# Performance work log

Measured on AMD Instinct MI355X. Metric: run time of the kernel, lower is better.

## Reference

```python
import jax, jax.numpy as jnp
import numpy as np


def setup_inputs() -> dict:
    key = jax.random.key(0)
    k1, k2, k3, k4 = jax.random.split(key, 4)
    B, T, C, H = 8, 2048, 1024, 64
    x = jax.random.normal(k1, (B, T, C), dtype=jnp.float32)
    Wq = jax.random.normal(k2, (C, H), dtype=jnp.float32) * (C ** -0.5)
    Wk = jax.random.normal(k3, (C, H), dtype=jnp.float32) * (C ** -0.5)
    Wv = jax.random.normal(k4, (C, H), dtype=jnp.float32) * (C ** -0.5)
    return {"x": x, "Wq": Wq, "Wk": Wk, "Wv": Wv}


def reference(x, Wq, Wk, Wv):
    # x: [B,T,C]; Wq/Wk/Wv: [C,H] (nn.Linear bias=False => x @ W)
    B, T, C = x.shape
    H = Wq.shape[-1]
    q = jnp.einsum('btc,ch->bth', x, Wq)
    k = jnp.einsum('btc,ch->bth', x, Wk)
    v = jnp.einsum('btc,ch->bth', x, Wv)
    scale = H ** -0.5
    att = jnp.einsum('bqh,bkh->bqk', q, k) * scale  # [B,T,T]
    causal = jnp.tril(jnp.ones((T, T), dtype=bool))
    att = jnp.where(causal, att, -jnp.inf)
    att = jax.nn.softmax(att, axis=-1)
    out = jnp.einsum('bqk,bkh->bqh', att, v)  # [B,T,H]
    return out
```

## Files before the change

kernel.cpp:

```cpp
#include <hip/hip_runtime.h>
#include <hip/hip_bf16.h>
#include <math.h>

#define BB 8
#define TT 2048
#define CC 1024
#define HH 64
#define BT (BB * TT)

typedef __attribute__((ext_vector_type(8))) short short8;
typedef __attribute__((ext_vector_type(4))) float floatx4;

static __device__ inline ushort f2bf(float f) {
    __hip_bfloat16 h = __float2bfloat16(f);
    return *reinterpret_cast<ushort*>(&h);
}
static __device__ inline unsigned int f2bf2(float lo, float hi) {
    __hip_bfloat162 h = __float22bfloat162_rn(make_float2(lo, hi));
    return *reinterpret_cast<unsigned int*>(&h);
}
static __device__ inline float bf2f(ushort u) {
    union { unsigned int i; float f; } c;
    c.i = ((unsigned int)u) << 16;
    return c.f;
}

__global__ __launch_bounds__(256) void wprep_kernel(
    const float* __restrict__ Wq, const float* __restrict__ Wk,
    const float* __restrict__ Wv, ushort* __restrict__ WbT)
{
    __shared__ float ws_[64 * 65];
    const int m  = blockIdx.x >> 4;
    const int kb = (blockIdx.x & 15) * 64;
    const float* W = (m == 0) ? Wq : (m == 1) ? Wk : Wv;
    const int t  = threadIdx.x;
    const int lr = t >> 4, lc = (t & 15) * 4;
    #pragma unroll
    for (int i = 0; i < 4; ++i) {
        const int row = lr + i * 16;
        float4 v = *(const float4*)&W[(size_t)(kb + row) * HH + lc];
        ws_[row * 65 + lc + 0] = v.x; ws_[row * 65 + lc + 1] = v.y;
        ws_[row * 65 + lc + 2] = v.z; ws_[row * 65 + lc + 3] = v.w;
    }
    __syncthreads();
    const int n = t & 63, kseg = t >> 6;
    union { ushort s[16]; uint4 q[2]; } u;
    #pragma unroll
    for (int j = 0; j < 16; ++j)
        u.s[j] = f2bf(ws_[(kseg * 16 + j) * 65 + n]);
    ushort* dst = &WbT[(size_t)(m * 64 + n) * 1024 + kb + kseg * 16];
    *(uint4*)&dst[0] = u.q[0];
    *(uint4*)&dst[8] = u.q[1];
}

__global__ __launch_bounds__(256, 2) void qkv_kernel(
    const float* __restrict__ x, const ushort* __restrict__ WbT,
    ushort* __restrict__ qb, ushort* __restrict__ kbS, ushort* __restrict__ vS)
{
    const int t    = threadIdx.x;
    const int w    = t >> 6;
    const int lane = t & 63;
    const int l16  = lane & 15;
    const int quad = lane >> 4;

    const int rows0 = blockIdx.x * 32 + (w >> 1) * 16;
    const int ct0   = (w & 1) * 6;

    const float* xr = &x[(size_t)(rows0 + l16) * CC + quad * 8];
    const ushort* wb = &WbT[(size_t)l16 * 1024 + quad * 8];

    floatx4 acc[6];
    #pragma unroll
    for (int c = 0; c < 6; ++c) acc[c] = (floatx4){0.f, 0.f, 0.f, 0.f};

    float4 xcA[2][2], xcB[2][2];
    #pragma unroll
    for (int p = 0; p < 2; ++p) {
        xcA[p][0] = *(const float4*)&xr[p * 32 + 0];
        xcA[p][1] = *(const float4*)&xr[p * 32 + 4];
        xcB[p][0] = *(const float4*)&xr[64 + p * 32 + 0];
        xcB[p][1] = *(const float4*)&xr[64 + p * 32 + 4];
    }

    short8 afA[2][6], afB[2][6];
    #pragma unroll
    for (int p = 0; p < 2; ++p)
        #pragma unroll
        for (int c = 0; c < 6; ++c)
            afA[p][c] = *(const short8*)&wb[(size_t)(ct0 + c) * 16384 + p * 32];

    auto body = [&](int it, float4 (&xc)[2][2], short8 (&aCur)[2][6], short8 (&aNxt)[2][6]) {
        short8 bx[2];
        #pragma unroll
        for (int p = 0; p < 2; ++p) {
            union { unsigned int u[4]; short8 s; } cv;
            cv.u[0] = f2bf2(xc[p][0].x, xc[p][0].y);
            cv.u[1] = f2bf2(xc[p][0].z, xc[p][0].w);
            cv.u[2] = f2bf2(xc[p][1].x, xc[p][1].y);
            cv.u[3] = f2bf2(xc[p][1].z, xc[p][1].w);
            bx[p] = cv.s;
        }
        if (it + 2 < 16) {
            #pragma unroll
            for (int p = 0; p < 2; ++p) {
                xc[p][0] = *(const float4*)&xr[(it + 2) * 64 + p * 32 + 0];
                xc[p][1] = *(const float4*)&xr[(it + 2) * 64 + p * 32 + 4];
            }
        }
        if (it + 1 < 16) {
            #pragma unroll
            for (int p = 0; p < 2; ++p)
                #pragma unroll
                for (int c = 0; c < 6; ++c)
                    aNxt[p][c] = *(const short8*)&wb[(size_t)(ct0 + c) * 16384
                                                     + (it + 1) * 64 + p * 32];
        }
        __builtin_amdgcn_s_setprio(1);
        #pragma unroll
        for (int p = 0; p < 2; ++p)
            #pragma unroll
            for (int c = 0; c < 6; ++c)
                acc[c] = __builtin_amdgcn_mfma_f32_16x16x32_bf16(aCur[p][c], bx[p], acc[c], 0, 0, 0);
        __builtin_amdgcn_s_setprio(0);
    };

    #pragma unroll 1
    for (int it2 = 0; it2 < 16; it2 += 4) {
        body(it2 + 0, xcA, afA, afB);
        body(it2 + 1, xcB, afB, afA);
        body(it2 + 2, xcA, afA, afB);
        body(it2 + 3, xcB, afB, afA);
    }

    const size_t tile = (size_t)(rows0 >> 6) * 4096;
    #pragma unroll
    for (int c = 0; c < 6; ++c) {
        const int ct    = ct0 + c;
        const int mtype = ct >> 2;
        const int nn    = ct & 3;
        if (mtype == 0) {
            uint2 u;
            u.x = f2bf2(acc[c][0] * 0.125f, acc[c][1] * 0.125f);
            u.y = f2bf2(acc[c][2] * 0.125f, acc[c][3] * 0.125f);
            *(uint2*)&qb[(size_t)(rows0 + l16) * HH + nn * 16 + quad * 4] = u;
        } else if (mtype == 1) {
            const int ckey  = (rows0 >> 4) & 3;
            const int p     = nn >> 1;
            const int quadP = (nn * 2 + (quad >> 1)) & 3;
            const int j0    = (quad & 1) * 4;
            uint2 u;
            u.x = f2bf2(acc[c][0], acc[c][1]);
            u.y = f2bf2(acc[c][2], acc[c][3]);
            *(uint2*)&kbS[tile + (size_t)((ckey * 2 + p) * 64 + quadP * 16 + l16) * 8 + j0] = u;
        } else {
            const int pv = (rows0 >> 5) & 1;
            const int qv = ((rows0 >> 4) & 1) * 2 + (l16 >> 3);
            const int jv = l16 & 7;
            #pragma unroll
            for (int reg = 0; reg < 4; ++reg)
                vS[tile + (size_t)((nn * 2 + pv) * 64 + qv * 16 + quad * 4 + reg) * 8 + jv]
                    = f2bf(acc[c][reg]);
        }
    }
}

__global__ __launch_bounds__(256) void attn_kernel(
    const ushort* __restrict__ qb, const ushort* __restrict__ kbS,
    const ushort* __restrict__ vS, ushort* __restrict__ Opart,
    float* __restrict__ ml)
{
    __shared__ __align__(16) ushort P[4][16 * 72];

    const int t    = threadIdx.x;
    const int w    = t >> 6;
    const int lane = t & 63;
    const int l16  = lane & 15;
    const int quad = lane >> 4;

    const int b   = blockIdx.x & 7;
    const int idx = blockIdx.x >> 3;
    int qt, part, np;
    if (idx < 32)      { qt = 31 - (idx >> 2); part = idx & 3; np = 4; }
    else if (idx < 56) { const int u = idx - 32; const int g = u / 3;
                         qt = 23 - g; part = u - g * 3; np = 3; }
    else if (idx < 72) { const int u = idx - 56; qt = 15 - (u >> 1); part = u & 1; np = 2; }
    else               { qt = 7 - (idx - 72); part = 0; np = 1; }
    const int ntiles = qt + 1;
    const int ktb = (part * ntiles) / np;
    const int kte = ((part + 1) * ntiles) / np;

    const ushort* ktile0 = kbS + (size_t)(b * 32) * 4096;
    const ushort* vtile0 = vS  + (size_t)(b * 32) * 4096;

    short8 qf[2];
    {
        const ushort* qrow = qb + ((size_t)b * TT + qt * 64 + w * 16) * HH;
        qf[0] = *(const short8*)&qrow[l16 * HH + quad * 8];
        qf[1] = *(const short8*)&qrow[l16 * HH + 32 + quad * 8];
    }
    short8 ones;
    #pragma unroll
    for (int i = 0; i < 8; ++i) ones[i] = (short)0x3F80;

    floatx4 o[4], osum;
    #pragma unroll
    for (int c = 0; c < 4; ++c) o[c] = (floatx4){0.f, 0.f, 0.f, 0.f};
    osum = (floatx4){0.f, 0.f, 0.f, 0.f};

    ushort* Pw = &P[w][0];

    for (int kt = ktb; kt < kte; ++kt) {
        const ushort* kg = ktile0 + (size_t)kt * 4096;
        const ushort* vg = vtile0 + (size_t)kt * 4096;

        short8 kf[4][2];
        #pragma unroll
        for (int c = 0; c < 4; ++c)
            #pragma unroll
            for (int p = 0; p < 2; ++p)
                kf[c][p] = *(const short8*)&kg[(size_t)(((c * 2 + p) * 64) + lane) * 8];

        floatx4 s[4];
        #pragma unroll
        for (int c = 0; c < 4; ++c) s[c] = (floatx4){0.f, 0.f, 0.f, 0.f};
        __builtin_amdgcn_s_setprio(1);
        #pragma unroll
        for (int c = 0; c < 4; ++c)
            #pragma unroll
            for (int p = 0; p < 2; ++p)
                s[c] = __builtin_amdgcn_mfma_f32_16x16x32_bf16(kf[c][p], qf[p], s[c], 0, 0, 0);
        __builtin_amdgcn_s_setprio(0);

        short8 vf[4][2];
        #pragma unroll
        for (int c = 0; c < 4; ++c)
            #pragma unroll
            for (int p = 0; p < 2; ++p)
                vf[c][p] = *(const short8*)&vg[(size_t)(((c * 2 + p) * 64) + lane) * 8];

        if (kt == ntiles - 1) {
            const int key0 = kt * 64 + quad * 4;
            const int qrow = qt * 64 + w * 16 + l16;
            #pragma unroll
            for (int c = 0; c < 4; ++c)
                #pragma unroll
                for (int reg = 0; reg < 4; ++reg)
                    if (key0 + c * 16 + reg > qrow) s[c][reg] = -1e30f;
        }

        #pragma unroll
        for (int c = 0; c < 4; ++c) {
            uint2 u;
            u.x = f2bf2(__expf(s[c][0]), __expf(s[c][1]));
            u.y = f2bf2(__expf(s[c][2]), __expf(s[c][3]));
            *(uint2*)&Pw[l16 * 72 + c * 16 + quad * 4] = u;
        }

        short8 pf[2];
        pf[0] = *(const short8*)&Pw[l16 * 72 + quad * 8];
        pf[1] = *(const short8*)&Pw[l16 * 72 + 32 + quad * 8];

        __builtin_amdgcn_s_setprio(1);
        #pragma unroll
        for (int p = 0; p < 2; ++p) {
            #pragma unroll
            for (int c = 0; c < 4; ++c)
                o[c] = __builtin_amdgcn_mfma_f32_16x16x32_bf16(pf[p], vf[c][p], o[c], 0, 0, 0);
            osum = __builtin_amdgcn_mfma_f32_16x16x32_bf16(pf[p], ones, osum, 0, 0, 0);
        }
        __builtin_amdgcn_s_setprio(0);
    }

    const size_t ub = (size_t)blockIdx.x * 4096;
    const int rbase = w * 16 + quad * 4;
    #pragma unroll
    for (int c = 0; c < 4; ++c) {
        uint2 u;
        u.x = f2bf2(o[c][0], o[c][1]);
        u.y = f2bf2(o[c][2], o[c][3]);
        *(uint2*)&Opart[ub + (size_t)(c * 16 + l16) * 64 + rbase] = u;
    }
    if (l16 == 0) {
        #pragma unroll
        for (int reg = 0; reg < 4; ++reg)
            ml[(size_t)blockIdx.x * 64 + rbase + reg] = osum[reg];
    }
}

__global__ __launch_bounds__(256) void merge_kernel(
    const ushort* __restrict__ Opart, const float* __restrict__ ml,
    float* __restrict__ out)
{
    const int t    = threadIdx.x;
    const int gw   = blockIdx.x * 4 + (t >> 6);
    const int lane = t & 63;
    const int b    = gw >> 8;
    const int v    = gw & 255;
    const int qt   = v >> 3;
    const int oct  = v & 7;

    int base, np;
    if (qt >= 24)      { base = (31 - qt) * 4;      np = 4; }
    else if (qt >= 16) { base = 32 + (23 - qt) * 3; np = 3; }
    else if (qt >= 8)  { base = 56 + (15 - qt) * 2; np = 2; }
    else               { base = 72 + (7 - qt);      np = 1; }

    float* obase = out + ((size_t)b * TT + qt * 64) * HH;

    #pragma unroll
    for (int rg = 0; rg < 2; ++rg) {
        const int row0 = oct * 8 + rg * 4;
        float dx = 0.f, dy = 0.f, dz = 0.f, dw = 0.f;
        float ax = 0.f, ay = 0.f, az = 0.f, aw = 0.f;
        for (int p = 0; p < np; ++p) {
            const int unit = (base + p) * 8 + b;
            float4 d = *(const float4*)&ml[(size_t)unit * 64 + row0];
            dx += d.x; dy += d.y; dz += d.z; dw += d.w;
            ushort4 ov = *(const ushort4*)&Opart[(size_t)unit * 4096 + lane * 64 + row0];
            ax += bf2f(ov.x); ay += bf2f(ov.y); az += bf2f(ov.z); aw += bf2f(ov.w);
        }
        obase[(size_t)(row0 + 0) * HH + lane] = ax / dx;
        obase[(size_t)(row0 + 1) * HH + lane] = ay / dy;
        obase[(size_t)(row0 + 2) * HH + lane] = az / dz;
        obase[(size_t)(row0 + 3) * HH + lane] = aw / dw;
    }
}

extern "C" void kernel_launch(void* const* d_in, const int* in_sizes, int n_in,
                              void* d_out, int out_size, void* d_ws, size_t ws_size,
                              hipStream_t stream)
{
    (void)in_sizes; (void)n_in; (void)out_size; (void)ws_size;
    const float* x  = (const float*)d_in[0];
    const float* Wq = (const float*)d_in[1];
    const float* Wk = (const float*)d_in[2];
    const float* Wv = (const float*)d_in[3];
    float* outp = (float*)d_out;

    char* base = (char*)d_ws;
    ushort* WbT   = (ushort*)(base);
    ushort* qbuf  = (ushort*)(base + 393216);
    ushort* kbS   = qbuf + (size_t)BT * HH;
    ushort* vSb   = kbS + (size_t)BT * HH;
    ushort* Opart = vSb + (size_t)BT * HH;
    float*  ml    = (float*)((char*)Opart + (size_t)640 * 4096 * 2);

    wprep_kernel<<<dim3(48),  256, 0, stream>>>(Wq, Wk, Wv, WbT);
    qkv_kernel  <<<dim3(512), 256, 0, stream>>>(x, WbT, qbuf, kbS, vSb);
    attn_kernel <<<dim3(640), 256, 0, stream>>>(qbuf, kbS, vSb, Opart, ml);
    merge_kernel<<<dim3(512), 256, 0, stream>>>(Opart, ml, outp);
}
```

Before: 165.2 us.

## Split QKV projection work across more blocks with fewer accumulators per wave

Each block of the QKV projection now covers 16 rows instead of 32, and each wave computes 3 column tiles instead of 6, so the grid doubles to 1024 blocks. The launch bound asks for 4 blocks per SM instead of 2. The explicit double-buffered register prefetch of weight fragments and the two-stage x prefetch are replaced by a simple loop that loads weights each iteration and prefetches x one step ahead. The aim is to hide memory latency through higher occupancy rather than software pipelining. The cost is that each x row is now read by four waves in one block instead of two, and the weights are read by twice as many blocks.

```diff
diff --git a/kernel.cpp b/kernel.cpp
--- a/kernel.cpp
+++ b/kernel.cpp
@@ -53,7 +53,7 @@
     *(uint4*)&dst[8] = u.q[1];
 }
 
-__global__ __launch_bounds__(256, 2) void qkv_kernel(
+__global__ __launch_bounds__(256, 4) void qkv_kernel(
     const float* __restrict__ x, const ushort* __restrict__ WbT,
     ushort* __restrict__ qb, ushort* __restrict__ kbS, ushort* __restrict__ vS)
 {
@@ -63,33 +63,33 @@
     const int l16  = lane & 15;
     const int quad = lane >> 4;
 
-    const int rows0 = blockIdx.x * 32 + (w >> 1) * 16;
-    const int ct0   = (w & 1) * 6;
+    const int rows0 = blockIdx.x * 16;
+    const int ct0   = w * 3;
 
     const float* xr = &x[(size_t)(rows0 + l16) * CC + quad * 8];
     const ushort* wb = &WbT[(size_t)l16 * 1024 + quad * 8];
 
-    floatx4 acc[6];
-    #pragma unroll
-    for (int c = 0; c < 6; ++c) acc[c] = (floatx4){0.f, 0.f, 0.f, 0.f};
-
-    float4 xcA[2][2], xcB[2][2];
+    floatx4 acc[3];
+    #pragma unroll
+    for (int c = 0; c < 3; ++c) acc[c] = (floatx4){0.f, 0.f, 0.f, 0.f};
+
+    float4 xc[2][2];
     #pragma unroll
     for (int p = 0; p < 2; ++p) {
-        xcA[p][0] = *(const float4*)&xr[p * 32 + 0];
-        xcA[p][1] = *(const float4*)&xr[p * 32 + 4];
-        xcB[p][0] = *(const float4*)&xr[64 + p * 32 + 0];
-        xcB[p][1] = *(const float4*)&xr[64 + p * 32 + 4];
-    }
-
-    short8 afA[2][6], afB[2][6];
-    #pragma unroll
-    for (int p = 0; p < 2; ++p)
-        #pragma unroll
-        for (int c = 0; c < 6; ++c)
-            afA[p][c] = *(const short8*)&wb[(size_t)(ct0 + c) * 16384 + p * 32];
-
-    auto body = [&](int it, float4 (&xc)[2][2], short8 (&aCur)[2][6], short8 (&aNxt)[2][6]) {
+        xc[p][0] = *(const float4*)&xr[p * 32 + 0];
+        xc[p][1] = *(const float4*)&xr[p * 32 + 4];
+    }
+
+    #pragma unroll 4
+    for (int it = 0; it < 16; ++it) {
+        short8 af[2][3];
+        #pragma unroll
+        for (int p = 0; p < 2; ++p)
+            #pragma unroll
+            for (int c = 0; c < 3; ++c)
+                af[p][c] = *(const short8*)&wb[(size_t)(ct0 + c) * 16384
+                                               + it * 64 + p * 32];
+
         short8 bx[2];
         #pragma unroll
         for (int p = 0; p < 2; ++p) {
@@ -100,41 +100,27 @@
             cv.u[3] = f2bf2(xc[p][1].z, xc[p][1].w);
             bx[p] = cv.s;
         }
-        if (it + 2 < 16) {
+
+        if (it + 1 < 16) {
             #pragma unroll
             for (int p = 0; p < 2; ++p) {
-                xc[p][0] = *(const float4*)&xr[(it + 2) * 64 + p * 32 + 0];
-                xc[p][1] = *(const float4*)&xr[(it + 2) * 64 + p * 32 + 4];
+                xc[p][0] = *(const float4*)&xr[(it + 1) * 64 + p * 32 + 0];
+                xc[p][1] = *(const float4*)&xr[(it + 1) * 64 + p * 32 + 4];
             }
         }
-        if (it + 1 < 16) {
-            #pragma unroll
-            for (int p = 0; p < 2; ++p)
-                #pragma unroll
-                for (int c = 0; c < 6; ++c)
-                    aNxt[p][c] = *(const short8*)&wb[(size_t)(ct0 + c) * 16384
-                                                     + (it + 1) * 64 + p * 32];
-        }
+
         __builtin_amdgcn_s_setprio(1);
         #pragma unroll
         for (int p = 0; p < 2; ++p)
             #pragma unroll
-            for (int c = 0; c < 6; ++c)
-                acc[c] = __builtin_amdgcn_mfma_f32_16x16x32_bf16(aCur[p][c], bx[p], acc[c], 0, 0, 0);
+            for (int c = 0; c < 3; ++c)
+                acc[c] = __builtin_amdgcn_mfma_f32_16x16x32_bf16(af[p][c], bx[p], acc[c], 0, 0, 0);
         __builtin_amdgcn_s_setprio(0);
-    };
-
-    #pragma unroll 1
-    for (int it2 = 0; it2 < 16; it2 += 4) {
-        body(it2 + 0, xcA, afA, afB);
-        body(it2 + 1, xcB, afB, afA);
-        body(it2 + 2, xcA, afA, afB);
-        body(it2 + 3, xcB, afB, afA);
     }
 
     const size_t tile = (size_t)(rows0 >> 6) * 4096;
     #pragma unroll
-    for (int c = 0; c < 6; ++c) {
+    for (int c = 0; c < 3; ++c) {
         const int ct    = ct0 + c;
         const int mtype = ct >> 2;
         const int nn    = ct & 3;
@@ -345,8 +331,8 @@
     ushort* Opart = vSb + (size_t)BT * HH;
     float*  ml    = (float*)((char*)Opart + (size_t)640 * 4096 * 2);
 
-    wprep_kernel<<<dim3(48),  256, 0, stream>>>(Wq, Wk, Wv, WbT);
-    qkv_kernel  <<<dim3(512), 256, 0, stream>>>(x, WbT, qbuf, kbS, vSb);
-    attn_kernel <<<dim3(640), 256, 0, stream>>>(qbuf, kbS, vSb, Opart, ml);
-    merge_kernel<<<dim3(512), 256, 0, stream>>>(Opart, ml, outp);
-}
+    wprep_kernel<<<dim3(48),   256, 0, stream>>>(Wq, Wk, Wv, WbT);
+    qkv_kernel  <<<dim3(1024), 256, 0, stream>>>(x, WbT, qbuf, kbS, vSb);
+    attn_kernel <<<dim3(640),  256, 0, stream>>>(qbuf, kbS, vSb, Opart, ml);
+    merge_kernel<<<dim3(512),  256, 0, stream>>>(Opart, ml, outp);
+}
```

Measured after the change: 179.4 us. +8.6%, slower.
